# Kernel tuning notes

Measured on AMD Instinct MI355X. Metric: run time of the kernel, lower is better.

## Reference

```python
import jax, jax.numpy as jnp
import numpy as np

TOP_K = 8
N_EXPERTS = 256
N_GROUP = 8
TOPK_GROUP = 4
SCALE = 2.5


def setup_inputs() -> dict:
    key = jax.random.key(0)
    k1, k2, k3 = jax.random.split(key, 3)
    hidden_states = jax.random.normal(k1, (4, 2048, 7168), dtype=jnp.float32)
    weight = jax.random.normal(k2, (N_EXPERTS, 7168), dtype=jnp.float32) * 0.02
    e_score_correction_bias = jax.random.normal(k3, (N_EXPERTS,), dtype=jnp.float32) * 0.1
    return {"hidden_states": hidden_states, "weight": weight,
            "e_score_correction_bias": e_score_correction_bias}


def reference(hidden_states, weight, e_score_correction_bias):
    B, S, H = hidden_states.shape
    x = hidden_states.reshape(-1, H).astype(jnp.float32)          # [T, H]
    router_logits = jnp.einsum('th,eh->te', x, weight)            # [T, E]
    scores = jax.nn.sigmoid(router_logits)                        # [T, E]
    scores_b = scores + e_score_correction_bias[None, :]          # bias-corrected
    T = x.shape[0]
    # per-group score = sum of top-2 bias-corrected scores in the group
    grouped = scores_b.reshape(T, N_GROUP, N_EXPERTS // N_GROUP)
    group_scores = jax.lax.top_k(grouped, 2)[0].sum(-1)           # [T, G]
    group_idx = jax.lax.top_k(group_scores, TOPK_GROUP)[1]        # [T, topk_group]
    group_mask = jax.nn.one_hot(group_idx, N_GROUP, dtype=jnp.bool_).any(axis=1)  # [T, G]
    expert_mask = jnp.repeat(group_mask, N_EXPERTS // N_GROUP, axis=-1)           # [T, E]
    masked = jnp.where(expert_mask, scores_b, -jnp.inf)
    _, topk_indices = jax.lax.top_k(masked, TOP_K)                # [T, top_k]
    topk_weights = jnp.take_along_axis(scores, topk_indices, axis=-1)  # un-biased scores
    topk_weights = topk_weights / jnp.sum(topk_weights, axis=-1, keepdims=True)
    topk_weights = topk_weights * SCALE
    return topk_indices, topk_weights
```

## Files before the change

kernel.cpp:

```cpp
#include <hip/hip_runtime.h>
#include <math.h>

typedef __attribute__((ext_vector_type(4))) float f32x4;
typedef _Float16 f16;
typedef __attribute__((ext_vector_type(8))) _Float16 f16x8;

constexpr int H       = 7168;
constexpr int E       = 256;
constexpr int T_TOTAL = 8192;

constexpr int KSPLIT  = 4;
constexpr int K_SLICE = H / KSPLIT;
constexpr int NCH     = K_SLICE / 64;
constexpr int MT      = 64;

constexpr int N_GROUP    = 8;
constexpr int TOPK_GROUP = 4;
constexpr int TOP_K      = 8;

constexpr size_t SCORES_OFF = 8u * 1024 * 1024;

__global__ __launch_bounds__(64) void pack_w_kernel(const float* __restrict__ w,
                                                    f16* __restrict__ wf)
{
    const int l  = threadIdx.x;
    const int nt = blockIdx.x & 15;
    const int kc = blockIdx.x >> 4;
    const int e  = nt * 16 + (l & 15);
    const int h  = kc * 32 + (l >> 4) * 8;
    const float* src = &w[(size_t)e * H + h];
    f32x4 v0 = *reinterpret_cast<const f32x4*>(src);
    f32x4 v1 = *reinterpret_cast<const f32x4*>(src + 4);
    float v[8] = {v0[0], v0[1], v0[2], v0[3], v1[0], v1[1], v1[2], v1[3]};
    f16x8 hi, lo;
    #pragma unroll
    for (int j = 0; j < 8; ++j) {
        f16 h16 = (f16)v[j];
        hi[j] = h16;
        lo[j] = (f16)(v[j] - (float)h16);
    }
    const size_t base = (((size_t)kc * 16 + nt) * 2) * 512 + (size_t)l * 8;
    *reinterpret_cast<f16x8*>(&wf[base])       = hi;
    *reinterpret_cast<f16x8*>(&wf[base + 512]) = lo;
}

__global__ __launch_bounds__(512, 4) void gemm_kernel(
    const float* __restrict__ x,
    const f16*   __restrict__ wf,
    float* __restrict__ scores)
{
    __shared__ __align__(16) f16 x_lds[2][4 * 2 * 2 * 512];

    const int tid  = threadIdx.x;
    const int lane = tid & 63;
    const int wn   = tid >> 6;

    const int bid = blockIdx.x;
    const int ksl = bid & 3;
    const int mb  = bid >> 2;
    const int t0  = mb * MT;
    const int k0  = ksl * K_SLICE;
    const int kc0 = k0 >> 5;

    const int lmt = (tid >> 6) & 3;
    const int lks = tid >> 8;
    const float* xrow = &x[(size_t)(t0 + lmt * 16 + (lane & 15)) * H
                           + k0 + lks * 32 + (lane >> 4) * 8];

    const int lm = lane & 15;
    const int kq = lane >> 4;

    f32x4 acc[4][2];
    #pragma unroll
    for (int mt = 0; mt < 4; ++mt)
        #pragma unroll
        for (int nt = 0; nt < 2; ++nt)
            acc[mt][nt] = (f32x4){0.f, 0.f, 0.f, 0.f};

    auto stage = [&](int buf, f32x4 v0, f32x4 v1) {
        float v[8] = {v0[0], v0[1], v0[2], v0[3], v1[0], v1[1], v1[2], v1[3]};
        f16x8 hi, lo;
        #pragma unroll
        for (int j = 0; j < 8; ++j) {
            f16 h16 = (f16)v[j];
            hi[j] = h16;
            lo[j] = (f16)(v[j] - (float)h16);
        }
        f16* base = &x_lds[buf][((lmt * 2 + lks) * 2) * 512 + lane * 8];
        *reinterpret_cast<f16x8*>(base)       = hi;
        *reinterpret_cast<f16x8*>(base + 512) = lo;
    };

    auto load_b = [&](f16x8 (&b)[2][2], int kc) {
        #pragma unroll
        for (int nt = 0; nt < 2; ++nt)
            #pragma unroll
            for (int s = 0; s < 2; ++s)
                b[nt][s] = *reinterpret_cast<const f16x8*>(
                    &wf[(((size_t)kc * 16 + wn * 2 + nt) * 2 + s) * 512 + lane * 8]);
    };

    auto mfma_step = [&](const f16x8 (&b)[2][2], int buf, int ks) {
        f16x8 a[4][2];
        #pragma unroll
        for (int mt = 0; mt < 4; ++mt)
            #pragma unroll
            for (int s = 0; s < 2; ++s)
                a[mt][s] = *reinterpret_cast<const f16x8*>(
                    &x_lds[buf][((mt * 2 + ks) * 2 + s) * 512 + lane * 8]);
        #pragma unroll
        for (int mt = 0; mt < 4; ++mt)
            #pragma unroll
            for (int nt = 0; nt < 2; ++nt)
                acc[mt][nt] = __builtin_amdgcn_mfma_f32_16x16x32_f16(
                    a[mt][0], b[nt][0], acc[mt][nt], 0, 0, 0);
        #pragma unroll
        for (int mt = 0; mt < 4; ++mt)
            #pragma unroll
            for (int nt = 0; nt < 2; ++nt)
                acc[mt][nt] = __builtin_amdgcn_mfma_f32_16x16x32_f16(
                    a[mt][0], b[nt][1], acc[mt][nt], 0, 0, 0);
        #pragma unroll
        for (int mt = 0; mt < 4; ++mt)
            #pragma unroll
            for (int nt = 0; nt < 2; ++nt)
                acc[mt][nt] = __builtin_amdgcn_mfma_f32_16x16x32_f16(
                    a[mt][1], b[nt][0], acc[mt][nt], 0, 0, 0);
    };

    f16x8 b0[2][2], b1[2][2];

    {
        f32x4 v0 = *reinterpret_cast<const f32x4*>(xrow);
        f32x4 v1 = *reinterpret_cast<const f32x4*>(xrow + 4);
        stage(0, v0, v1);
    }
    load_b(b0, kc0);
    __syncthreads();

    for (int ch = 0; ch < NCH; ++ch) {
        const int buf = ch & 1;
        f32x4 nv0, nv1;
        if (ch + 1 < NCH) {
            const float* nx = xrow + (ch + 1) * 64;
            nv0 = *reinterpret_cast<const f32x4*>(nx);
            nv1 = *reinterpret_cast<const f32x4*>(nx + 4);
        }
        load_b(b1, kc0 + ch * 2 + 1);
        mfma_step(b0, buf, 0);
        load_b(b0, (ch + 1 < NCH) ? (kc0 + (ch + 1) * 2) : kc0);
        mfma_step(b1, buf, 1);

        if (ch + 1 < NCH) stage(buf ^ 1, nv0, nv1);
        __syncthreads();
    }

    #pragma unroll
    for (int mt = 0; mt < 4; ++mt)
        #pragma unroll
        for (int nt = 0; nt < 2; ++nt)
            #pragma unroll
            for (int r = 0; r < 4; ++r) {
                const int tok = mt * 16 + kq * 4 + r;
                const int e   = wn * 32 + nt * 16 + lm;
                scores[(((size_t)(t0 + tok)) * KSPLIT + ksl) * E + e] = acc[mt][nt][r];
            }
}

__global__ __launch_bounds__(256) void gate_kernel(
    const float* __restrict__ scores,
    const float* __restrict__ bias,
    float* __restrict__ out)
{
    const int lane = threadIdx.x & 63;
    const int wv   = threadIdx.x >> 6;
    const int t    = blockIdx.x * 4 + wv;

    const float* p = &scores[(size_t)t * (KSPLIT * E) + lane * 4];
    f32x4 s = (f32x4){0.f, 0.f, 0.f, 0.f};
    #pragma unroll
    for (int k = 0; k < KSPLIT; ++k)
        s += *reinterpret_cast<const f32x4*>(p + k * E);
    f32x4 bi = *reinterpret_cast<const f32x4*>(&bias[lane * 4]);

    float sig[4], bsc[4];
    #pragma unroll
    for (int j = 0; j < 4; ++j) {
        sig[j] = 1.0f / (1.0f + expf(-s[j]));
        bsc[j] = sig[j] + bi[j];
    }

    float h01 = fmaxf(bsc[0], bsc[1]), l01 = fminf(bsc[0], bsc[1]);
    float h23 = fmaxf(bsc[2], bsc[3]), l23 = fminf(bsc[2], bsc[3]);
    float m1 = fmaxf(h01, h23);
    float m2 = fmaxf(fminf(h01, h23), fmaxf(l01, l23));
    #pragma unroll
    for (int d = 1; d < 8; d <<= 1) {
        float om1 = __shfl_xor(m1, d);
        float om2 = __shfl_xor(m2, d);
        float nm1 = fmaxf(m1, om1);
        float nm2 = fmaxf(fminf(m1, om1), fmaxf(m2, om2));
        m1 = nm1; m2 = nm2;
    }
    const float gs  = m1 + m2;
    const int   gid = lane >> 3;

    int cnt = 0;
    #pragma unroll
    for (int j = 0; j < N_GROUP; ++j) {
        float gsj = __shfl(gs, j * 8);
        cnt += (gsj > gs || (gsj == gs && j < gid)) ? 1 : 0;
    }
    const bool sel = (cnt < TOPK_GROUP);

    float mb[4];
    #pragma unroll
    for (int j = 0; j < 4; ++j) mb[j] = sel ? bsc[j] : -INFINITY;

    float wsum = 0.f;
    f32x4 iv0, iv1, wv0, wv1;
    #pragma unroll
    for (int r = 0; r < TOP_K; ++r) {
        float v = mb[0]; int li = 0;
        if (mb[1] > v) { v = mb[1]; li = 1; }
        if (mb[2] > v) { v = mb[2]; li = 2; }
        if (mb[3] > v) { v = mb[3]; li = 3; }
        int ei = lane * 4 + li;
        #pragma unroll
        for (int d = 1; d < 64; d <<= 1) {
            float ov = __shfl_xor(v, d);
            int   oi = __shfl_xor(ei, d);
            if (ov > v || (ov == v && oi < ei)) { v = ov; ei = oi; }
        }
        const int sub = ei & 3, owner = ei >> 2;
        const float svl = (sub & 2) ? ((sub & 1) ? sig[3] : sig[2])
                                    : ((sub & 1) ? sig[1] : sig[0]);
        const float wr = __shfl(svl, owner);
        #pragma unroll
        for (int j = 0; j < 4; ++j)
            if (lane == owner && j == sub) mb[j] = -INFINITY;
        wsum += wr;
        if (r < 4) { iv0[r] = (float)ei;     wv0[r] = wr; }
        else       { iv1[r - 4] = (float)ei; wv1[r - 4] = wr; }
    }

    const float scale = 2.5f / wsum;
    #pragma unroll
    for (int j = 0; j < 4; ++j) { wv0[j] *= scale; wv1[j] *= scale; }

    if (lane == 0) {
        float* oi_ = out + (size_t)t * TOP_K;
        float* ow_ = out + (size_t)T_TOTAL * TOP_K + (size_t)t * TOP_K;
        *reinterpret_cast<f32x4*>(oi_)     = iv0;
        *reinterpret_cast<f32x4*>(oi_ + 4) = iv1;
        *reinterpret_cast<f32x4*>(ow_)     = wv0;
        *reinterpret_cast<f32x4*>(ow_ + 4) = wv1;
    }
}

extern "C" void kernel_launch(void* const* d_in, const int* in_sizes, int n_in,
                              void* d_out, int out_size, void* d_ws, size_t ws_size,
                              hipStream_t stream) {
    const float* x    = (const float*)d_in[0];
    const float* w    = (const float*)d_in[1];
    const float* bias = (const float*)d_in[2];
    float* out = (float*)d_out;

    f16*   wf     = (f16*)d_ws;
    float* scores = (float*)((char*)d_ws + SCORES_OFF);

    hipLaunchKernelGGL(pack_w_kernel, dim3((H / 32) * 16), dim3(64), 0, stream, w, wf);
    hipLaunchKernelGGL(gemm_kernel, dim3((T_TOTAL / MT) * KSPLIT), dim3(512), 0, stream,
                       x, wf, scores);
    hipLaunchKernelGGL(gate_kernel, dim3(T_TOTAL / 4), dim3(256), 0, stream,
                       scores, bias, out);
}
```

Before: 369.1 us.

## Process two K-chunks per barrier and interleave LDS loads with MFMAs

```diff
diff --git a/kernel.cpp b/kernel.cpp
--- a/kernel.cpp
+++ b/kernel.cpp
@@ -12,6 +12,7 @@
 constexpr int KSPLIT  = 4;
 constexpr int K_SLICE = H / KSPLIT;
 constexpr int NCH     = K_SLICE / 64;
+constexpr int NPAIR   = NCH / 2;
 constexpr int MT      = 64;
 
 constexpr int N_GROUP    = 8;
@@ -49,7 +50,7 @@
     const f16*   __restrict__ wf,
     float* __restrict__ scores)
 {
-    __shared__ __align__(16) f16 x_lds[2][4 * 2 * 2 * 512];
+    __shared__ __align__(16) f16 x_lds[2][2][4 * 2 * 2 * 512];
 
     const int tid  = threadIdx.x;
     const int lane = tid & 63;
@@ -77,7 +78,7 @@
         for (int nt = 0; nt < 2; ++nt)
             acc[mt][nt] = (f32x4){0.f, 0.f, 0.f, 0.f};
 
-    auto stage = [&](int buf, f32x4 v0, f32x4 v1) {
+    auto stage = [&](int bu, int half, f32x4 v0, f32x4 v1) {
         float v[8] = {v0[0], v0[1], v0[2], v0[3], v1[0], v1[1], v1[2], v1[3]};
         f16x8 hi, lo;
         #pragma unroll
@@ -86,7 +87,7 @@
             hi[j] = h16;
             lo[j] = (f16)(v[j] - (float)h16);
         }
-        f16* base = &x_lds[buf][((lmt * 2 + lks) * 2) * 512 + lane * 8];
+        f16* base = &x_lds[bu][half][((lmt * 2 + lks) * 2) * 512 + lane * 8];
         *reinterpret_cast<f16x8*>(base)       = hi;
         *reinterpret_cast<f16x8*>(base + 512) = lo;
     };
@@ -100,32 +101,19 @@
                     &wf[(((size_t)kc * 16 + wn * 2 + nt) * 2 + s) * 512 + lane * 8]);
     };
 
-    auto mfma_step = [&](const f16x8 (&b)[2][2], int buf, int ks) {
-        f16x8 a[4][2];
-        #pragma unroll
-        for (int mt = 0; mt < 4; ++mt)
-            #pragma unroll
-            for (int s = 0; s < 2; ++s)
-                a[mt][s] = *reinterpret_cast<const f16x8*>(
-                    &x_lds[buf][((mt * 2 + ks) * 2 + s) * 512 + lane * 8]);
-        #pragma unroll
-        for (int mt = 0; mt < 4; ++mt)
-            #pragma unroll
-            for (int nt = 0; nt < 2; ++nt)
-                acc[mt][nt] = __builtin_amdgcn_mfma_f32_16x16x32_f16(
-                    a[mt][0], b[nt][0], acc[mt][nt], 0, 0, 0);
-        #pragma unroll
-        for (int mt = 0; mt < 4; ++mt)
-            #pragma unroll
-            for (int nt = 0; nt < 2; ++nt)
-                acc[mt][nt] = __builtin_amdgcn_mfma_f32_16x16x32_f16(
-                    a[mt][0], b[nt][1], acc[mt][nt], 0, 0, 0);
-        #pragma unroll
-        for (int mt = 0; mt < 4; ++mt)
-            #pragma unroll
-            for (int nt = 0; nt < 2; ++nt)
-                acc[mt][nt] = __builtin_amdgcn_mfma_f32_16x16x32_f16(
-                    a[mt][1], b[nt][0], acc[mt][nt], 0, 0, 0);
+    auto mfma_step = [&](const f16x8 (&b)[2][2], int bu, int half, int ks) {
+        #pragma unroll
+        for (int mt = 0; mt < 4; ++mt) {
+            const f16* ap = &x_lds[bu][half][((mt * 2 + ks) * 2) * 512 + lane * 8];
+            f16x8 ahi = *reinterpret_cast<const f16x8*>(ap);
+            f16x8 alo = *reinterpret_cast<const f16x8*>(ap + 512);
+            acc[mt][0] = __builtin_amdgcn_mfma_f32_16x16x32_f16(ahi, b[0][0], acc[mt][0], 0, 0, 0);
+            acc[mt][1] = __builtin_amdgcn_mfma_f32_16x16x32_f16(ahi, b[1][0], acc[mt][1], 0, 0, 0);
+            acc[mt][0] = __builtin_amdgcn_mfma_f32_16x16x32_f16(ahi, b[0][1], acc[mt][0], 0, 0, 0);
+            acc[mt][1] = __builtin_amdgcn_mfma_f32_16x16x32_f16(ahi, b[1][1], acc[mt][1], 0, 0, 0);
+            acc[mt][0] = __builtin_amdgcn_mfma_f32_16x16x32_f16(alo, b[0][0], acc[mt][0], 0, 0, 0);
+            acc[mt][1] = __builtin_amdgcn_mfma_f32_16x16x32_f16(alo, b[1][0], acc[mt][1], 0, 0, 0);
+        }
     };
 
     f16x8 b0[2][2], b1[2][2];
@@ -133,26 +121,46 @@
     {
         f32x4 v0 = *reinterpret_cast<const f32x4*>(xrow);
         f32x4 v1 = *reinterpret_cast<const f32x4*>(xrow + 4);
-        stage(0, v0, v1);
+        f32x4 v2 = *reinterpret_cast<const f32x4*>(xrow + 64);
+        f32x4 v3 = *reinterpret_cast<const f32x4*>(xrow + 68);
+        stage(0, 0, v0, v1);
+        stage(0, 1, v2, v3);
     }
     load_b(b0, kc0);
     __syncthreads();
 
-    for (int ch = 0; ch < NCH; ++ch) {
-        const int buf = ch & 1;
-        f32x4 nv0, nv1;
-        if (ch + 1 < NCH) {
-            const float* nx = xrow + (ch + 1) * 64;
-            nv0 = *reinterpret_cast<const f32x4*>(nx);
-            nv1 = *reinterpret_cast<const f32x4*>(nx + 4);
-        }
-        load_b(b1, kc0 + ch * 2 + 1);
-        mfma_step(b0, buf, 0);
-        load_b(b0, (ch + 1 < NCH) ? (kc0 + (ch + 1) * 2) : kc0);
-        mfma_step(b1, buf, 1);
-
-        if (ch + 1 < NCH) stage(buf ^ 1, nv0, nv1);
-        __syncthreads();
+    for (int i = 0; i < NPAIR; ++i) {
+        const int buf   = i & 1;
+        const int kbase = kc0 + i * 4;
+        const bool last = (i + 1 == NPAIR);
+
+        f32x4 nva0, nva1, nvb0, nvb1;
+        if (!last) {
+            const float* nx = xrow + (2 * i + 2) * 64;
+            nva0 = *reinterpret_cast<const f32x4*>(nx);
+            nva1 = *reinterpret_cast<const f32x4*>(nx + 4);
+            nvb0 = *reinterpret_cast<const f32x4*>(nx + 64);
+            nvb1 = *reinterpret_cast<const f32x4*>(nx + 68);
+        }
+
+        load_b(b1, kbase + 1);
+        __builtin_amdgcn_s_setprio(1);
+        mfma_step(b0, buf, 0, 0);
+        load_b(b0, kbase + 2);
+        mfma_step(b1, buf, 0, 1);
+        load_b(b1, kbase + 3);
+        mfma_step(b0, buf, 1, 0);
+        load_b(b0, last ? kc0 : (kbase + 4));
+        mfma_step(b1, buf, 1, 1);
+        __builtin_amdgcn_s_setprio(0);
+
+        if (!last) {
+            stage(buf ^ 1, 0, nva0, nva1);
+            stage(buf ^ 1, 1, nvb0, nvb1);
+            asm volatile("s_waitcnt lgkmcnt(0)" ::: "memory");
+            __builtin_amdgcn_s_barrier();
+            asm volatile("" ::: "memory");
+        }
     }
 
     #pragma unroll
```

Measured after the change: 372.1 us. No clear change (+0.8%).
